# Optimization experiments

Hardware: AMD Instinct MI355X
Metric: run time of the kernel (lower is better)

The kernel has to match this reference:

```python
import jax, jax.numpy as jnp
import numpy as np

N_NODES = 50000
N_EDGES = 600000
DIM = 128
N_LAYERS = 2


def setup_inputs() -> dict:
    key = jax.random.key(0)
    ks = jax.random.split(key, 4)
    x = jax.random.normal(ks[0], (N_NODES, DIM), dtype=jnp.float32)
    edge_index = jax.random.randint(ks[1], (2, N_EDGES), 0, N_NODES, dtype=jnp.int32)
    # xavier_normal-ish scale for transform (fan_in=fan_out=DIM) and gate
    Wt = jax.random.normal(ks[2], (N_LAYERS, DIM, DIM), dtype=jnp.float32) * (1.414 * (2.0 / (2 * DIM)) ** 0.5)
    Wg = jax.random.normal(ks[3], (N_LAYERS, DIM), dtype=jnp.float32) * (1.414 * (2.0 / (DIM + 1)) ** 0.5)
    bt = jnp.zeros((N_LAYERS, DIM), dtype=jnp.float32)
    bg = jnp.zeros((N_LAYERS,), dtype=jnp.float32)
    return {"x": x, "edge_index": edge_index, "Wt": Wt, "bt": bt, "Wg": Wg, "bg": bg}


def _fa_layer(h, row, col, Wt_l, bt_l, Wg_l, bg_l):
    # h: [N, D]. transform
    h = h @ Wt_l.T + bt_l
    n = h.shape[0]
    ones = jnp.ones(row.shape, dtype=h.dtype)
    deg = jnp.clip(jax.ops.segment_sum(ones, row, num_segments=n), 1.0)
    dinv = deg ** -0.5  # [N]
    # per-edge gate on source node features
    g = jnp.tanh(h[row] @ Wg_l + bg_l)  # [E]
    norm = g * dinv[row] * dinv[col]    # [E]
    msg = norm[:, None] * h[row]        # [E, D]
    out = jax.ops.segment_sum(msg, col, num_segments=n)
    return out + h


def reference(x, edge_index, Wt, bt, Wg, bg):
    row, col = edge_index[0], edge_index[1]
    h = x
    for l in range(N_LAYERS):
        h = _fa_layer(h, row, col, Wt[l], bt[l], Wg[l], bg[l])
        h = jax.nn.relu(h)  # dropout p=0 / eval -> identity
    return h
```

## Files before the change

kernel.cpp:

```cpp
#include <hip/hip_runtime.h>
#include <cstdint>
#include <cstddef>

#define DIM 128
#define BM 128
#define NB1 128
#define RBITS 14
#define RSIZE (1 << RBITS)
#define NB2 32
#define NWC 4

typedef __attribute__((ext_vector_type(8))) short bf16x8;
typedef __attribute__((ext_vector_type(16))) float f32x16;

__device__ inline unsigned short f2b(float x) {
    unsigned int u = __float_as_uint(x);
    unsigned int r = (u + 0x7fffu + ((u >> 16) & 1u)) >> 16;
    return (unsigned short)r;
}
__device__ inline float blo(unsigned int u) { return __uint_as_float(u << 16); }
__device__ inline float bhi(unsigned int u) { return __uint_as_float(u & 0xffff0000u); }

__global__ __launch_bounds__(256) void hists_kernel(
    const int* __restrict__ row, const int* __restrict__ col,
    const float* __restrict__ Wt, unsigned short* __restrict__ wbuf,
    int* __restrict__ gcounts, int* __restrict__ counts,
    int E, int ndeg, int nbuk, int bshift)
{
    __shared__ int hs[RSIZE];
    int b = blockIdx.x;
    if (b < ndeg) {
        int r = b / NB2, bi = b % NB2;
        for (int i = threadIdx.x; i < RSIZE; i += 256) hs[i] = 0;
        __syncthreads();
        int chunk = (E + NB2 - 1) / NB2;
        int e0 = bi * chunk, e1 = min(E, e0 + chunk);
        for (int e = e0 + threadIdx.x; e < e1; e += 256) {
            int rv = row[e];
            if ((rv >> RBITS) == r) atomicAdd(&hs[rv & (RSIZE - 1)], 1);
        }
        __syncthreads();
        int* outp = gcounts + (size_t)b * RSIZE;
        for (int i = threadIdx.x; i < RSIZE; i += 256) outp[i] = hs[i];
    } else if (b < ndeg + NB1) {
        int hb = b - ndeg;
        for (int i = threadIdx.x; i < nbuk; i += 256) hs[i] = 0;
        __syncthreads();
        int chunk = (E + NB1 - 1) / NB1;
        int e0 = hb * chunk, e1 = min(E, e0 + chunk);
        for (int e = e0 + threadIdx.x; e < e1; e += 256)
            atomicAdd(&hs[col[e] >> bshift], 1);
        __syncthreads();
        int* outp = counts + (size_t)hb * nbuk;
        for (int i = threadIdx.x; i < nbuk; i += 256) outp[i] = hs[i];
    } else {
        int b2 = b - ndeg - NB1;
#pragma unroll
        for (int k = 0; k < 4; ++k) {
            int idx = b2 * 1024 + k * 256 + threadIdx.x;
            int L = idx >> 11;
            int rem = idx & 2047;
            int r = rem >> 4;
            int cc = rem & 15;
            const float* src = Wt + (size_t)L * DIM * DIM + r * DIM + cc * 8;
            float4 v0 = *(const float4*)(src);
            float4 v1 = *(const float4*)(src + 4);
            unsigned short o[8];
            o[0] = f2b(v0.x); o[1] = f2b(v0.y); o[2] = f2b(v0.z); o[3] = f2b(v0.w);
            o[4] = f2b(v1.x); o[5] = f2b(v1.y); o[6] = f2b(v1.z); o[7] = f2b(v1.w);
            unsigned short* dst = wbuf + (size_t)L * DIM * DIM + r * DIM + (cc ^ (r & 15)) * 8;
            *(int4*)dst = *(const int4*)o;
        }
    }
}

__global__ __launch_bounds__(256) void scan_dinv_kernel(
    int* __restrict__ counts, int* __restrict__ tot,
    const int* __restrict__ gcounts, float* __restrict__ dinv,
    int nbuk, int n, int nscan)
{
    int b = blockIdx.x;
    if (b < nscan) {
        int w = threadIdx.x >> 6;
        int lane = threadIdx.x & 63;
        int t = b * 4 + w;
        if (t >= nbuk) return;
        int c0 = counts[(size_t)(lane * 2) * nbuk + t];
        int c1 = counts[(size_t)(lane * 2 + 1) * nbuk + t];
        int s = c0 + c1;
        int x = s;
#pragma unroll
        for (int d = 1; d < 64; d <<= 1) {
            int y = __shfl_up(x, (unsigned)d, 64);
            if (lane >= d) x += y;
        }
        int excl = x - s;
        counts[(size_t)(lane * 2) * nbuk + t] = excl;
        counts[(size_t)(lane * 2 + 1) * nbuk + t] = excl + c0;
        if (lane == 63) tot[t] = x;
    } else {
        int i = (b - nscan) * 256 + threadIdx.x;
        if (i >= n) return;
        int r = i >> RBITS, bl = i & (RSIZE - 1);
        int s = 0;
        for (int bi = 0; bi < NB2; ++bi)
            s += gcounts[(size_t)(r * NB2 + bi) * RSIZE + bl];
        dinv[i] = rsqrtf((float)max(s, 1));
    }
}

__global__ __launch_bounds__(256) void scatter_kernel(
    const int* __restrict__ row, const int* __restrict__ col,
    const int* __restrict__ bases, const int* __restrict__ tot,
    unsigned int* __restrict__ tmp, int* __restrict__ bstart,
    int E, int nbuk, int bshift)
{
    __shared__ int scanbuf[256];
    __shared__ int bst[1024];
    __shared__ int cur[1024];
    int t = threadIdx.x;
    int v[4];
    int s = 0;
#pragma unroll
    for (int k = 0; k < 4; ++k) {
        int idx = t * 4 + k;
        v[k] = (idx < nbuk) ? tot[idx] : 0;
        s += v[k];
    }
    scanbuf[t] = s;
    __syncthreads();
    for (int d = 1; d < 256; d <<= 1) {
        int y = (t >= d) ? scanbuf[t - d] : 0;
        __syncthreads();
        scanbuf[t] += y;
        __syncthreads();
    }
    int run = scanbuf[t] - s;
#pragma unroll
    for (int k = 0; k < 4; ++k) {
        int idx = t * 4 + k;
        if (idx < nbuk) bst[idx] = run;
        run += v[k];
    }
    __syncthreads();
    const int* mybase = bases + (size_t)blockIdx.x * nbuk;
    for (int i = t; i < nbuk; i += 256) cur[i] = bst[i] + mybase[i];
    if (blockIdx.x == 0) {
        for (int i = t; i < nbuk; i += 256) bstart[i] = bst[i];
        if (t == 0) bstart[nbuk] = E;
    }
    __syncthreads();
    int chunk = (E + NB1 - 1) / NB1;
    int e0 = blockIdx.x * chunk, e1 = min(E, e0 + chunk);
    int rsh = 32 - bshift;
    unsigned int smask = (1u << bshift) - 1u;
    for (int e = e0 + t; e < e1; e += 256) {
        int c = col[e];
        int pos = atomicAdd(&cur[c >> bshift], 1);
        tmp[pos] = (((unsigned int)c & smask) << rsh) | (unsigned int)row[e];
    }
}

__global__ __launch_bounds__(256) void bucket_group_kernel(
    const unsigned int* __restrict__ tmp, const int* __restrict__ bstart,
    int* __restrict__ off, int* __restrict__ csr, int n, int E, int bshift)
{
    __shared__ int subh[4096];
    const int b = blockIdx.x;
    const int tid = threadIdx.x;
    const int subb = 1 << bshift;
    const int rsh = 32 - bshift;
    const unsigned int rmask = (1u << rsh) - 1u;
    int beg = bstart[b], end = bstart[b + 1];

    for (int i = tid; i < subb; i += 256) subh[i] = 0;
    __syncthreads();
    for (int i = beg + tid; i < end; i += 256)
        atomicAdd(&subh[tmp[i] >> rsh], 1);
    __syncthreads();
    if (subb <= 64) {
        if (tid < 64) {
            int v = (tid < subb) ? subh[tid] : 0;
            int x = v;
            for (int d = 1; d < 64; d <<= 1) {
                int y = __shfl_up(x, (unsigned)d, 64);
                if (tid >= d) x += y;
            }
            if (tid < subb) subh[tid] = x - v;
        }
    } else {
        if (tid == 0) {
            int run = 0;
            for (int i = 0; i < subb; ++i) { int c = subh[i]; subh[i] = run; run += c; }
        }
    }
    __syncthreads();
    int c0 = b << bshift;
    for (int i = tid; i < subb; i += 256) {
        int c = c0 + i;
        if (c < n) off[c] = beg + subh[i];
    }
    if (b == gridDim.x - 1 && tid == 0) off[n] = E;
    __syncthreads();
    for (int i = beg + tid; i < end; i += 256) {
        unsigned int v = tmp[i];
        int rank = atomicAdd(&subh[v >> rsh], 1);
        csr[beg + rank] = (int)(v & rmask);
    }
}

template <bool BF16IN>
__global__ __launch_bounds__(256) void transform_kernel(
    const void* __restrict__ hin_v, const unsigned short* __restrict__ wbuf,
    const float* __restrict__ bt, const float* __restrict__ Wg,
    const float* __restrict__ bg, const float* __restrict__ dinv,
    unsigned short* __restrict__ h1b, float* __restrict__ aout, int n)
{
    __shared__ __align__(16) unsigned short h_s[BM * DIM];
    __shared__ __align__(16) unsigned short w_s[DIM * DIM];
    __shared__ float p_s[BM];

    const int tid = threadIdx.x;
    const int node0 = blockIdx.x * BM;
    const int lane = tid & 63;
    const int wv = tid >> 6;

#pragma unroll
    for (int it = 0; it < 8; ++it) {
        int g = it * 256 + tid;
        ((int4*)w_s)[g] = ((const int4*)wbuf)[g];
    }
    if constexpr (BF16IN) {
        const int4* hin = (const int4*)hin_v;
#pragma unroll
        for (int it = 0; it < 8; ++it) {
            int g = it * 256 + tid;
            int r = g >> 4;
            int src = node0 + r;
            if (src >= n) src = n - 1;
            ((int4*)h_s)[g] = hin[(size_t)src * 16 + (g & 15)];
        }
    } else {
        const float* hin = (const float*)hin_v;
#pragma unroll
        for (int it = 0; it < 16; ++it) {
            int g = it * 256 + tid;
            int r = g >> 5;
            int c4 = g & 31;
            int src = node0 + r;
            if (src >= n) src = n - 1;
            float4 hv = *(const float4*)(hin + (size_t)src * DIM + c4 * 4);
            int chunk = (c4 >> 1) ^ (r & 15);
            int base = r * DIM + chunk * 8 + (c4 & 1) * 4;
            h_s[base + 0] = f2b(hv.x); h_s[base + 1] = f2b(hv.y);
            h_s[base + 2] = f2b(hv.z); h_s[base + 3] = f2b(hv.w);
        }
    }
    __syncthreads();

    f32x16 acc[4] = {};
    const int l31 = lane & 31;
    const int asel = lane >> 5;
    const int swz = l31 & 15;
    const unsigned short* ha = h_s + (wv * 32 + l31) * DIM;
#pragma unroll
    for (int ks = 0; ks < 8; ++ks) {
        int ch = ((ks * 2 + asel) ^ swz) * 8;
        bf16x8 av = *(const bf16x8*)(ha + ch);
#pragma unroll
        for (int cf = 0; cf < 4; ++cf) {
            bf16x8 bv = *(const bf16x8*)(w_s + (cf * 32 + l31) * DIM + ch);
            acc[cf] = __builtin_amdgcn_mfma_f32_32x32x16_bf16(av, bv, acc[cf], 0, 0, 0);
        }
    }
    __syncthreads();

    float btc[4], wgc[4];
#pragma unroll
    for (int cf = 0; cf < 4; ++cf) {
        btc[cf] = bt[cf * 32 + l31];
        wgc[cf] = Wg[cf * 32 + l31];
    }
    float p[16];
#pragma unroll
    for (int q = 0; q < 16; ++q) p[q] = 0.0f;
#pragma unroll
    for (int cf = 0; cf < 4; ++cf) {
#pragma unroll
        for (int q = 0; q < 16; ++q) {
            float v = acc[cf][q] + btc[cf];
            p[q] = fmaf(v, wgc[cf], p[q]);
            int row = (q & 3) + 8 * (q >> 2) + 4 * asel;
            h_s[(wv * 32 + row) * DIM + cf * 32 + l31] = f2b(v);
        }
    }
#pragma unroll
    for (int m = 1; m < 32; m <<= 1) {
#pragma unroll
        for (int q = 0; q < 16; ++q) p[q] += __shfl_xor(p[q], m, 64);
    }
    if (l31 == 0) {
#pragma unroll
        for (int q = 0; q < 16; ++q) {
            int row = (q & 3) + 8 * (q >> 2) + 4 * asel;
            p_s[wv * 32 + row] = p[q];
        }
    }
    __syncthreads();

#pragma unroll
    for (int it = 0; it < 8; ++it) {
        int g = it * 256 + tid;
        int r = g >> 4;
        int c = g & 15;
        int4 v = *(const int4*)(h_s + r * DIM + c * 8);
        int dst = node0 + r;
        if (dst < n) *(int4*)(h1b + (size_t)dst * DIM + c * 8) = v;
    }

    if (tid < BM) {
        int node = node0 + tid;
        if (node < n) aout[node] = tanhf(p_s[tid] + bg[0]) * dinv[node];
    }
}

template <bool BF16OUT>
__global__ __launch_bounds__(256) void agg_kernel(
    const int* __restrict__ off, const int* __restrict__ csr_row,
    const float* __restrict__ a, const float* __restrict__ dinv,
    const unsigned short* __restrict__ h1b, void* __restrict__ out_v, int n)
{
    int node = blockIdx.x * 4 + (threadIdx.x >> 6);
    if (node >= n) return;
    int lane = threadIdx.x & 63;
    int beg = off[node], end = off[node + 1];
    const unsigned int* hb = (const unsigned int*)h1b;
    float s0x = 0.f, s0y = 0.f, s1x = 0.f, s1y = 0.f;
    float s2x = 0.f, s2y = 0.f, s3x = 0.f, s3y = 0.f;
    int s = beg;
    for (; s + 4 <= end; s += 4) {
        int r0 = csr_row[s], r1 = csr_row[s + 1], r2 = csr_row[s + 2], r3 = csr_row[s + 3];
        float a0 = a[r0], a1 = a[r1], a2 = a[r2], a3 = a[r3];
        unsigned int u0 = hb[(size_t)r0 * 64 + lane];
        unsigned int u1 = hb[(size_t)r1 * 64 + lane];
        unsigned int u2 = hb[(size_t)r2 * 64 + lane];
        unsigned int u3 = hb[(size_t)r3 * 64 + lane];
        s0x = fmaf(a0, blo(u0), s0x); s0y = fmaf(a0, bhi(u0), s0y);
        s1x = fmaf(a1, blo(u1), s1x); s1y = fmaf(a1, bhi(u1), s1y);
        s2x = fmaf(a2, blo(u2), s2x); s2y = fmaf(a2, bhi(u2), s2y);
        s3x = fmaf(a3, blo(u3), s3x); s3y = fmaf(a3, bhi(u3), s3y);
    }
    for (; s < end; ++s) {
        int r0 = csr_row[s];
        float a0 = a[r0];
        unsigned int u0 = hb[(size_t)r0 * 64 + lane];
        s0x = fmaf(a0, blo(u0), s0x); s0y = fmaf(a0, bhi(u0), s0y);
    }
    float dv = dinv[node];
    unsigned int ur = hb[(size_t)node * 64 + lane];
    float ox = fmaxf(fmaf(dv, s0x + s1x + s2x + s3x, blo(ur)), 0.0f);
    float oy = fmaxf(fmaf(dv, s0y + s1y + s2y + s3y, bhi(ur)), 0.0f);
    if constexpr (BF16OUT) {
        unsigned int pk = (unsigned int)f2b(ox) | ((unsigned int)f2b(oy) << 16);
        int pos = (((lane >> 2) ^ (node & 15)) << 2) + (lane & 3);
        ((unsigned int*)out_v)[(size_t)node * 64 + pos] = pk;
    } else {
        ((float2*)out_v)[(size_t)node * 64 + lane] = make_float2(ox, oy);
    }
}

extern "C" void kernel_launch(void* const* d_in, const int* in_sizes, int n_in,
                              void* d_out, int out_size, void* d_ws, size_t ws_size,
                              hipStream_t stream) {
    const float* x    = (const float*)d_in[0];
    const int*   edge = (const int*)d_in[1];
    const float* Wt   = (const float*)d_in[2];
    const float* bt   = (const float*)d_in[3];
    const float* Wg   = (const float*)d_in[4];
    const float* bg   = (const float*)d_in[5];
    float* out = (float*)d_out;

    const int n = in_sizes[0] / DIM;
    const int E = in_sizes[1] / 2;
    const int* row = edge;
    const int* col = edge + E;

    int bshift = 6;
    while (((n + (1 << bshift) - 1) >> bshift) > 1024) ++bshift;
    const int nbuk = (n + (1 << bshift) - 1) >> bshift;
    const int nr = (n + RSIZE - 1) >> RBITS;
    const int ndeg = nr * NB2;

    char* base = (char*)d_ws;
    size_t o = 0;
    auto carve = [&](size_t bytes) -> void* {
        void* p = base + o;
        o += (bytes + 255) & ~(size_t)255;
        return p;
    };
    unsigned short* h1b  = (unsigned short*)carve((size_t)n * DIM * 2);
    unsigned short* hbuf = (unsigned short*)carve((size_t)n * DIM * 2);
    unsigned short* wbuf = (unsigned short*)carve((size_t)2 * DIM * DIM * 2);
    float* dinv          = (float*)carve((size_t)n * 4);
    float* a             = (float*)carve((size_t)n * 4);
    int*   off           = (int*)carve((size_t)(n + 1) * 4);
    int*   csr           = (int*)carve((size_t)E * 4);
    unsigned int* tmp    = (unsigned int*)carve((size_t)E * 4);
    int*   counts        = (int*)carve((size_t)NB1 * nbuk * 4);
    int*   bstart        = (int*)carve((size_t)(nbuk + 1) * 4);
    int*   tot           = (int*)carve((size_t)nbuk * 4);
    int*   gcounts       = (int*)carve((size_t)ndeg * RSIZE * 4);

    hists_kernel<<<ndeg + NB1 + NWC, 256, 0, stream>>>(
        row, col, Wt, wbuf, gcounts, counts, E, ndeg, nbuk, bshift);
    const int nscan = (nbuk + 3) / 4;
    const int ndinv = (n + 255) / 256;
    scan_dinv_kernel<<<nscan + ndinv, 256, 0, stream>>>(counts, tot, gcounts, dinv,
                                                        nbuk, n, nscan);
    scatter_kernel<<<NB1, 256, 0, stream>>>(row, col, counts, tot, tmp, bstart,
                                            E, nbuk, bshift);
    bucket_group_kernel<<<nbuk, 256, 0, stream>>>(tmp, bstart, off, csr, n, E, bshift);

    const int gt = (n + BM - 1) / BM;
    const int ga = (n + 3) / 4;

    transform_kernel<false><<<gt, 256, 0, stream>>>(
        x, wbuf, bt, Wg, bg, dinv, h1b, a, n);
    agg_kernel<true><<<ga, 256, 0, stream>>>(off, csr, a, dinv, h1b, hbuf, n);

    transform_kernel<true><<<gt, 256, 0, stream>>>(
        hbuf, wbuf + DIM * DIM, bt + DIM, Wg + DIM, bg + 1, dinv, h1b, a, n);
    agg_kernel<false><<<ga, 256, 0, stream>>>(off, csr, a, dinv, h1b, out, n);
}
```

Baseline: 150.0 us.

## Fold layer-1 transform into histogram kernel and defer gate epilogue

The first-layer dense transform now runs as extra blocks of the histogram/weight-conversion kernel. Those blocks convert Wt from fp32 on the fly and store the raw gate pre-activation, since dinv is not yet available at that point. The tanh*dinv gate is finished by extra blocks appended to the scatter kernel. This removes one launch and overlaps the GEMM with the CSR build. Aggregation outputs now use nontemporal stores. The cost is a larger shared-memory footprint for all blocks in the merged kernel, which may reduce histogram-block occupancy.

```diff
diff --git a/kernel.cpp b/kernel.cpp
--- a/kernel.cpp
+++ b/kernel.cpp
@@ -21,216 +21,47 @@
 __device__ inline float blo(unsigned int u) { return __uint_as_float(u << 16); }
 __device__ inline float bhi(unsigned int u) { return __uint_as_float(u & 0xffff0000u); }
 
-__global__ __launch_bounds__(256) void hists_kernel(
-    const int* __restrict__ row, const int* __restrict__ col,
-    const float* __restrict__ Wt, unsigned short* __restrict__ wbuf,
-    int* __restrict__ gcounts, int* __restrict__ counts,
-    int E, int ndeg, int nbuk, int bshift)
+struct GArgs {
+    const float* x; const int* row; const int* col;
+    const float* Wt; const float* bt; const float* Wg; const float* bg;
+    unsigned short* wbuf; unsigned short* h1b; unsigned short* hbuf;
+    float* dinv; float* a; float* praw; float* out;
+    int* off; int* csr; unsigned int* tmp; int* counts; int* bstart; int* tot;
+    int* gcounts;
+    int n, E, nbuk, bshift, ndeg, nscan, ndinv, gt, ga;
+};
+
+__device__ void transform_body(bool bf16in, bool wfromf32, const void* hin_v,
+    const float* WtL, const unsigned short* wbufL,
+    const float* btL, const float* WgL, float bgL,
+    const float* dinv, unsigned short* h1b, float* aout, bool fullepi,
+    int n, int tb, unsigned short* h_s, unsigned short* w_s, float* p_s)
 {
-    __shared__ int hs[RSIZE];
-    int b = blockIdx.x;
-    if (b < ndeg) {
-        int r = b / NB2, bi = b % NB2;
-        for (int i = threadIdx.x; i < RSIZE; i += 256) hs[i] = 0;
-        __syncthreads();
-        int chunk = (E + NB2 - 1) / NB2;
-        int e0 = bi * chunk, e1 = min(E, e0 + chunk);
-        for (int e = e0 + threadIdx.x; e < e1; e += 256) {
-            int rv = row[e];
-            if ((rv >> RBITS) == r) atomicAdd(&hs[rv & (RSIZE - 1)], 1);
-        }
-        __syncthreads();
-        int* outp = gcounts + (size_t)b * RSIZE;
-        for (int i = threadIdx.x; i < RSIZE; i += 256) outp[i] = hs[i];
-    } else if (b < ndeg + NB1) {
-        int hb = b - ndeg;
-        for (int i = threadIdx.x; i < nbuk; i += 256) hs[i] = 0;
-        __syncthreads();
-        int chunk = (E + NB1 - 1) / NB1;
-        int e0 = hb * chunk, e1 = min(E, e0 + chunk);
-        for (int e = e0 + threadIdx.x; e < e1; e += 256)
-            atomicAdd(&hs[col[e] >> bshift], 1);
-        __syncthreads();
-        int* outp = counts + (size_t)hb * nbuk;
-        for (int i = threadIdx.x; i < nbuk; i += 256) outp[i] = hs[i];
-    } else {
-        int b2 = b - ndeg - NB1;
-#pragma unroll
-        for (int k = 0; k < 4; ++k) {
-            int idx = b2 * 1024 + k * 256 + threadIdx.x;
-            int L = idx >> 11;
-            int rem = idx & 2047;
-            int r = rem >> 4;
-            int cc = rem & 15;
-            const float* src = Wt + (size_t)L * DIM * DIM + r * DIM + cc * 8;
-            float4 v0 = *(const float4*)(src);
-            float4 v1 = *(const float4*)(src + 4);
-            unsigned short o[8];
-            o[0] = f2b(v0.x); o[1] = f2b(v0.y); o[2] = f2b(v0.z); o[3] = f2b(v0.w);
-            o[4] = f2b(v1.x); o[5] = f2b(v1.y); o[6] = f2b(v1.z); o[7] = f2b(v1.w);
-            unsigned short* dst = wbuf + (size_t)L * DIM * DIM + r * DIM + (cc ^ (r & 15)) * 8;
-            *(int4*)dst = *(const int4*)o;
-        }
-    }
-}
-
-__global__ __launch_bounds__(256) void scan_dinv_kernel(
-    int* __restrict__ counts, int* __restrict__ tot,
-    const int* __restrict__ gcounts, float* __restrict__ dinv,
-    int nbuk, int n, int nscan)
-{
-    int b = blockIdx.x;
-    if (b < nscan) {
-        int w = threadIdx.x >> 6;
-        int lane = threadIdx.x & 63;
-        int t = b * 4 + w;
-        if (t >= nbuk) return;
-        int c0 = counts[(size_t)(lane * 2) * nbuk + t];
-        int c1 = counts[(size_t)(lane * 2 + 1) * nbuk + t];
-        int s = c0 + c1;
-        int x = s;
-#pragma unroll
-        for (int d = 1; d < 64; d <<= 1) {
-            int y = __shfl_up(x, (unsigned)d, 64);
-            if (lane >= d) x += y;
-        }
-        int excl = x - s;
-        counts[(size_t)(lane * 2) * nbuk + t] = excl;
-        counts[(size_t)(lane * 2 + 1) * nbuk + t] = excl + c0;
-        if (lane == 63) tot[t] = x;
-    } else {
-        int i = (b - nscan) * 256 + threadIdx.x;
-        if (i >= n) return;
-        int r = i >> RBITS, bl = i & (RSIZE - 1);
-        int s = 0;
-        for (int bi = 0; bi < NB2; ++bi)
-            s += gcounts[(size_t)(r * NB2 + bi) * RSIZE + bl];
-        dinv[i] = rsqrtf((float)max(s, 1));
-    }
-}
-
-__global__ __launch_bounds__(256) void scatter_kernel(
-    const int* __restrict__ row, const int* __restrict__ col,
-    const int* __restrict__ bases, const int* __restrict__ tot,
-    unsigned int* __restrict__ tmp, int* __restrict__ bstart,
-    int E, int nbuk, int bshift)
-{
-    __shared__ int scanbuf[256];
-    __shared__ int bst[1024];
-    __shared__ int cur[1024];
-    int t = threadIdx.x;
-    int v[4];
-    int s = 0;
-#pragma unroll
-    for (int k = 0; k < 4; ++k) {
-        int idx = t * 4 + k;
-        v[k] = (idx < nbuk) ? tot[idx] : 0;
-        s += v[k];
-    }
-    scanbuf[t] = s;
-    __syncthreads();
-    for (int d = 1; d < 256; d <<= 1) {
-        int y = (t >= d) ? scanbuf[t - d] : 0;
-        __syncthreads();
-        scanbuf[t] += y;
-        __syncthreads();
-    }
-    int run = scanbuf[t] - s;
-#pragma unroll
-    for (int k = 0; k < 4; ++k) {
-        int idx = t * 4 + k;
-        if (idx < nbuk) bst[idx] = run;
-        run += v[k];
-    }
-    __syncthreads();
-    const int* mybase = bases + (size_t)blockIdx.x * nbuk;
-    for (int i = t; i < nbuk; i += 256) cur[i] = bst[i] + mybase[i];
-    if (blockIdx.x == 0) {
-        for (int i = t; i < nbuk; i += 256) bstart[i] = bst[i];
-        if (t == 0) bstart[nbuk] = E;
-    }
-    __syncthreads();
-    int chunk = (E + NB1 - 1) / NB1;
-    int e0 = blockIdx.x * chunk, e1 = min(E, e0 + chunk);
-    int rsh = 32 - bshift;
-    unsigned int smask = (1u << bshift) - 1u;
-    for (int e = e0 + t; e < e1; e += 256) {
-        int c = col[e];
-        int pos = atomicAdd(&cur[c >> bshift], 1);
-        tmp[pos] = (((unsigned int)c & smask) << rsh) | (unsigned int)row[e];
-    }
-}
-
-__global__ __launch_bounds__(256) void bucket_group_kernel(
-    const unsigned int* __restrict__ tmp, const int* __restrict__ bstart,
-    int* __restrict__ off, int* __restrict__ csr, int n, int E, int bshift)
-{
-    __shared__ int subh[4096];
-    const int b = blockIdx.x;
     const int tid = threadIdx.x;
-    const int subb = 1 << bshift;
-    const int rsh = 32 - bshift;
-    const unsigned int rmask = (1u << rsh) - 1u;
-    int beg = bstart[b], end = bstart[b + 1];
-
-    for (int i = tid; i < subb; i += 256) subh[i] = 0;
-    __syncthreads();
-    for (int i = beg + tid; i < end; i += 256)
-        atomicAdd(&subh[tmp[i] >> rsh], 1);
-    __syncthreads();
-    if (subb <= 64) {
-        if (tid < 64) {
-            int v = (tid < subb) ? subh[tid] : 0;
-            int x = v;
-            for (int d = 1; d < 64; d <<= 1) {
-                int y = __shfl_up(x, (unsigned)d, 64);
-                if (tid >= d) x += y;
-            }
-            if (tid < subb) subh[tid] = x - v;
-        }
-    } else {
-        if (tid == 0) {
-            int run = 0;
-            for (int i = 0; i < subb; ++i) { int c = subh[i]; subh[i] = run; run += c; }
-        }
-    }
-    __syncthreads();
-    int c0 = b << bshift;
-    for (int i = tid; i < subb; i += 256) {
-        int c = c0 + i;
-        if (c < n) off[c] = beg + subh[i];
-    }
-    if (b == gridDim.x - 1 && tid == 0) off[n] = E;
-    __syncthreads();
-    for (int i = beg + tid; i < end; i += 256) {
-        unsigned int v = tmp[i];
-        int rank = atomicAdd(&subh[v >> rsh], 1);
-        csr[beg + rank] = (int)(v & rmask);
-    }
-}
-
-template <bool BF16IN>
-__global__ __launch_bounds__(256) void transform_kernel(
-    const void* __restrict__ hin_v, const unsigned short* __restrict__ wbuf,
-    const float* __restrict__ bt, const float* __restrict__ Wg,
-    const float* __restrict__ bg, const float* __restrict__ dinv,
-    unsigned short* __restrict__ h1b, float* __restrict__ aout, int n)
-{
-    __shared__ __align__(16) unsigned short h_s[BM * DIM];
-    __shared__ __align__(16) unsigned short w_s[DIM * DIM];
-    __shared__ float p_s[BM];
-
-    const int tid = threadIdx.x;
-    const int node0 = blockIdx.x * BM;
+    const int node0 = tb * BM;
     const int lane = tid & 63;
     const int wv = tid >> 6;
 
-#pragma unroll
-    for (int it = 0; it < 8; ++it) {
-        int g = it * 256 + tid;
-        ((int4*)w_s)[g] = ((const int4*)wbuf)[g];
-    }
-    if constexpr (BF16IN) {
+    if (wfromf32) {
+#pragma unroll
+        for (int it = 0; it < 16; ++it) {
+            int g = it * 256 + tid;
+            int r = g >> 5;
+            int c4 = g & 31;
+            int chunk = (c4 >> 1) ^ (r & 15);
+            int base = r * DIM + chunk * 8 + (c4 & 1) * 4;
+            float4 wvv = *(const float4*)(WtL + (size_t)r * DIM + c4 * 4);
+            w_s[base + 0] = f2b(wvv.x); w_s[base + 1] = f2b(wvv.y);
+            w_s[base + 2] = f2b(wvv.z); w_s[base + 3] = f2b(wvv.w);
+        }
+    } else {
+#pragma unroll
+        for (int it = 0; it < 8; ++it) {
+            int g = it * 256 + tid;
+            ((int4*)w_s)[g] = ((const int4*)wbufL)[g];
+        }
+    }
+    if (bf16in) {
         const int4* hin = (const int4*)hin_v;
 #pragma unroll
         for (int it = 0; it < 8; ++it) {
@@ -278,8 +109,8 @@
     float btc[4], wgc[4];
 #pragma unroll
     for (int cf = 0; cf < 4; ++cf) {
-        btc[cf] = bt[cf * 32 + l31];
-        wgc[cf] = Wg[cf * 32 + l31];
+        btc[cf] = btL[cf * 32 + l31];
+        wgc[cf] = WgL[cf * 32 + l31];
     }
     float p[16];
 #pragma unroll
@@ -290,8 +121,8 @@
         for (int q = 0; q < 16; ++q) {
             float v = acc[cf][q] + btc[cf];
             p[q] = fmaf(v, wgc[cf], p[q]);
-            int row = (q & 3) + 8 * (q >> 2) + 4 * asel;
-            h_s[(wv * 32 + row) * DIM + cf * 32 + l31] = f2b(v);
+            int rr = (q & 3) + 8 * (q >> 2) + 4 * asel;
+            h_s[(wv * 32 + rr) * DIM + cf * 32 + l31] = f2b(v);
         }
     }
 #pragma unroll
@@ -302,8 +133,8 @@
     if (l31 == 0) {
 #pragma unroll
         for (int q = 0; q < 16; ++q) {
-            int row = (q & 3) + 8 * (q >> 2) + 4 * asel;
-            p_s[wv * 32 + row] = p[q];
+            int rr = (q & 3) + 8 * (q >> 2) + 4 * asel;
+            p_s[wv * 32 + rr] = p[q];
         }
     }
     __syncthreads();
@@ -320,27 +151,221 @@
 
     if (tid < BM) {
         int node = node0 + tid;
-        if (node < n) aout[node] = tanhf(p_s[tid] + bg[0]) * dinv[node];
-    }
+        if (node < n) {
+            if (fullepi) aout[node] = tanhf(p_s[tid] + bgL) * dinv[node];
+            else         aout[node] = p_s[tid];
+        }
+    }
+}
+
+__global__ __launch_bounds__(256) void mega1_kernel(GArgs A) {
+    __shared__ __align__(16) unsigned char smem[66048];
+    int b = blockIdx.x;
+    if (b < A.ndeg) {
+        int* hs = (int*)smem;
+        int r = b / NB2, bi = b % NB2;
+        for (int i = threadIdx.x; i < RSIZE; i += 256) hs[i] = 0;
+        __syncthreads();
+        int chunk = (A.E + NB2 - 1) / NB2;
+        int e0 = bi * chunk, e1 = min(A.E, e0 + chunk);
+        for (int e = e0 + threadIdx.x; e < e1; e += 256) {
+            int rv = A.row[e];
+            if ((rv >> RBITS) == r) atomicAdd(&hs[rv & (RSIZE - 1)], 1);
+        }
+        __syncthreads();
+        int* outp = A.gcounts + (size_t)b * RSIZE;
+        for (int i = threadIdx.x; i < RSIZE; i += 256) outp[i] = hs[i];
+    } else if (b < A.ndeg + NB1) {
+        int* hs = (int*)smem;
+        int hb = b - A.ndeg;
+        for (int i = threadIdx.x; i < A.nbuk; i += 256) hs[i] = 0;
+        __syncthreads();
+        int chunk = (A.E + NB1 - 1) / NB1;
+        int e0 = hb * chunk, e1 = min(A.E, e0 + chunk);
+        for (int e = e0 + threadIdx.x; e < e1; e += 256)
+            atomicAdd(&hs[A.col[e] >> A.bshift], 1);
+        __syncthreads();
+        int* outp = A.counts + (size_t)hb * A.nbuk;
+        for (int i = threadIdx.x; i < A.nbuk; i += 256) outp[i] = hs[i];
+    } else if (b < A.ndeg + NB1 + NWC) {
+        int b2 = b - A.ndeg - NB1;
+#pragma unroll
+        for (int k = 0; k < 4; ++k) {
+            int idx = b2 * 1024 + k * 256 + threadIdx.x;
+            int L = idx >> 11;
+            int rem = idx & 2047;
+            int r = rem >> 4;
+            int cc = rem & 15;
+            const float* src = A.Wt + (size_t)L * DIM * DIM + r * DIM + cc * 8;
+            float4 v0 = *(const float4*)(src);
+            float4 v1 = *(const float4*)(src + 4);
+            unsigned short o[8];
+            o[0] = f2b(v0.x); o[1] = f2b(v0.y); o[2] = f2b(v0.z); o[3] = f2b(v0.w);
+            o[4] = f2b(v1.x); o[5] = f2b(v1.y); o[6] = f2b(v1.z); o[7] = f2b(v1.w);
+            unsigned short* dst = A.wbuf + (size_t)L * DIM * DIM + r * DIM + (cc ^ (r & 15)) * 8;
+            *(int4*)dst = *(const int4*)o;
+        }
+    } else {
+        int tb = b - (A.ndeg + NB1 + NWC);
+        unsigned short* h_s = (unsigned short*)smem;
+        unsigned short* w_s = h_s + BM * DIM;
+        float* p_s = (float*)(w_s + DIM * DIM);
+        transform_body(false, true, A.x, A.Wt, nullptr, A.bt, A.Wg, 0.0f,
+                       nullptr, A.h1b, A.praw, false, A.n, tb, h_s, w_s, p_s);
+    }
+}
+
+__global__ __launch_bounds__(256) void scan_dinv_kernel(GArgs A) {
+    int b = blockIdx.x;
+    if (b < A.nscan) {
+        int w = threadIdx.x >> 6;
+        int lane = threadIdx.x & 63;
+        int t = b * 4 + w;
+        if (t >= A.nbuk) return;
+        int c0 = A.counts[(size_t)(lane * 2) * A.nbuk + t];
+        int c1 = A.counts[(size_t)(lane * 2 + 1) * A.nbuk + t];
+        int s = c0 + c1;
+        int x = s;
+#pragma unroll
+        for (int d = 1; d < 64; d <<= 1) {
+            int y = __shfl_up(x, (unsigned)d, 64);
+            if (lane >= d) x += y;
+        }
+        int excl = x - s;
+        A.counts[(size_t)(lane * 2) * A.nbuk + t] = excl;
+        A.counts[(size_t)(lane * 2 + 1) * A.nbuk + t] = excl + c0;
+        if (lane == 63) A.tot[t] = x;
+    } else {
+        int i = (b - A.nscan) * 256 + threadIdx.x;
+        if (i >= A.n) return;
+        int r = i >> RBITS, bl = i & (RSIZE - 1);
+        int s = 0;
+        for (int bi = 0; bi < NB2; ++bi)
+            s += A.gcounts[(size_t)(r * NB2 + bi) * RSIZE + bl];
+        A.dinv[i] = rsqrtf((float)max(s, 1));
+    }
+}
+
+__global__ __launch_bounds__(256) void scatter_kernel(GArgs A) {
+    int b = blockIdx.x;
+    int t = threadIdx.x;
+    if (b >= NB1) {
+        int i = (b - NB1) * 256 + t;
+        if (i < A.n) A.a[i] = tanhf(A.praw[i] + A.bg[0]) * A.dinv[i];
+        return;
+    }
+    __shared__ int scanbuf[256];
+    __shared__ int bst[1024];
+    __shared__ int cur[1024];
+    int v[4];
+    int s = 0;
+#pragma unroll
+    for (int k = 0; k < 4; ++k) {
+        int idx = t * 4 + k;
+        v[k] = (idx < A.nbuk) ? A.tot[idx] : 0;
+        s += v[k];
+    }
+    scanbuf[t] = s;
+    __syncthreads();
+    for (int d = 1; d < 256; d <<= 1) {
+        int y = (t >= d) ? scanbuf[t - d] : 0;
+        __syncthreads();
+        scanbuf[t] += y;
+        __syncthreads();
+    }
+    int run = scanbuf[t] - s;
+#pragma unroll
+    for (int k = 0; k < 4; ++k) {
+        int idx = t * 4 + k;
+        if (idx < A.nbuk) bst[idx] = run;
+        run += v[k];
+    }
+    __syncthreads();
+    const int* mybase = A.counts + (size_t)b * A.nbuk;
+    for (int i = t; i < A.nbuk; i += 256) cur[i] = bst[i] + mybase[i];
+    if (b == 0) {
+        for (int i = t; i < A.nbuk; i += 256) A.bstart[i] = bst[i];
+        if (t == 0) A.bstart[A.nbuk] = A.E;
+    }
+    __syncthreads();
+    int chunk = (A.E + NB1 - 1) / NB1;
+    int e0 = b * chunk, e1 = min(A.E, e0 + chunk);
+    int rsh = 32 - A.bshift;
+    unsigned int smask = (1u << A.bshift) - 1u;
+    for (int e = e0 + t; e < e1; e += 256) {
+        int c = A.col[e];
+        int pos = atomicAdd(&cur[c >> A.bshift], 1);
+        A.tmp[pos] = (((unsigned int)c & smask) << rsh) | (unsigned int)A.row[e];
+    }
+}
+
+__global__ __launch_bounds__(256) void bucket_group_kernel(GArgs A) {
+    __shared__ int subh[4096];
+    const int b = blockIdx.x;
+    const int tid = threadIdx.x;
+    const int subb = 1 << A.bshift;
+    const int rsh = 32 - A.bshift;
+    const unsigned int rmask = (1u << rsh) - 1u;
+    int beg = A.bstart[b], end = A.bstart[b + 1];
+
+    for (int i = tid; i < subb; i += 256) subh[i] = 0;
+    __syncthreads();
+    for (int i = beg + tid; i < end; i += 256)
+        atomicAdd(&subh[A.tmp[i] >> rsh], 1);
+    __syncthreads();
+    if (subb <= 64) {
+        if (tid < 64) {
+            int v = (tid < subb) ? subh[tid] : 0;
+            int x = v;
+            for (int d = 1; d < 64; d <<= 1) {
+                int y = __shfl_up(x, (unsigned)d, 64);
+                if (tid >= d) x += y;
+            }
+            if (tid < subb) subh[tid] = x - v;
+        }
+    } else {
+        if (tid == 0) {
+            int run = 0;
+            for (int i = 0; i < subb; ++i) { int c = subh[i]; subh[i] = run; run += c; }
+        }
+    }
+    __syncthreads();
+    int c0 = b << A.bshift;
+    for (int i = tid; i < subb; i += 256) {
+        int c = c0 + i;
+        if (c < A.n) A.off[c] = beg + subh[i];
+    }
+    if (b == (int)gridDim.x - 1 && tid == 0) A.off[A.n] = A.E;
+    __syncthreads();
+    for (int i = beg + tid; i < end; i += 256) {
+        unsigned int v = A.tmp[i];
+        int rank = atomicAdd(&subh[v >> rsh], 1);
+        A.csr[beg + rank] = (int)(v & rmask);
+    }
+}
+
+__global__ __launch_bounds__(256) void t1_kernel(GArgs A) {
+    __shared__ __align__(16) unsigned short h_s[BM * DIM];
+    __shared__ __align__(16) unsigned short w_s[DIM * DIM];
+    __shared__ float p_s[BM];
+    transform_body(true, false, A.hbuf, nullptr, A.wbuf + DIM * DIM,
+                   A.bt + DIM, A.Wg + DIM, A.bg[1], A.dinv, A.h1b, A.a, true,
+                   A.n, blockIdx.x, h_s, w_s, p_s);
 }
 
 template <bool BF16OUT>
-__global__ __launch_bounds__(256) void agg_kernel(
-    const int* __restrict__ off, const int* __restrict__ csr_row,
-    const float* __restrict__ a, const float* __restrict__ dinv,
-    const unsigned short* __restrict__ h1b, void* __restrict__ out_v, int n)
-{
+__global__ __launch_bounds__(256) void agg_kernel(GArgs A, void* out_v) {
     int node = blockIdx.x * 4 + (threadIdx.x >> 6);
-    if (node >= n) return;
+    if (node >= A.n) return;
     int lane = threadIdx.x & 63;
-    int beg = off[node], end = off[node + 1];
-    const unsigned int* hb = (const unsigned int*)h1b;
+    int beg = A.off[node], end = A.off[node + 1];
+    const unsigned int* hb = (const unsigned int*)A.h1b;
     float s0x = 0.f, s0y = 0.f, s1x = 0.f, s1y = 0.f;
     float s2x = 0.f, s2y = 0.f, s3x = 0.f, s3y = 0.f;
     int s = beg;
     for (; s + 4 <= end; s += 4) {
-        int r0 = csr_row[s], r1 = csr_row[s + 1], r2 = csr_row[s + 2], r3 = csr_row[s + 3];
-        float a0 = a[r0], a1 = a[r1], a2 = a[r2], a3 = a[r3];
+        int r0 = A.csr[s], r1 = A.csr[s + 1], r2 = A.csr[s + 2], r3 = A.csr[s + 3];
+        float a0 = A.a[r0], a1 = A.a[r1], a2 = A.a[r2], a3 = A.a[r3];
         unsigned int u0 = hb[(size_t)r0 * 64 + lane];
         unsigned int u1 = hb[(size_t)r1 * 64 + lane];
         unsigned int u2 = hb[(size_t)r2 * 64 + lane];
@@ -351,21 +376,23 @@
         s3x = fmaf(a3, blo(u3), s3x); s3y = fmaf(a3, bhi(u3), s3y);
     }
     for (; s < end; ++s) {
-        int r0 = csr_row[s];
-        float a0 = a[r0];
+        int r0 = A.csr[s];
+        float a0 = A.a[r0];
         unsigned int u0 = hb[(size_t)r0 * 64 + lane];
         s0x = fmaf(a0, blo(u0), s0x); s0y = fmaf(a0, bhi(u0), s0y);
     }
-    float dv = dinv[node];
+    float dv = A.dinv[node];
     unsigned int ur = hb[(size_t)node * 64 + lane];
     float ox = fmaxf(fmaf(dv, s0x + s1x + s2x + s3x, blo(ur)), 0.0f);
     float oy = fmaxf(fmaf(dv, s0y + s1y + s2y + s3y, bhi(ur)), 0.0f);
     if constexpr (BF16OUT) {
         unsigned int pk = (unsigned int)f2b(ox) | ((unsigned int)f2b(oy) << 16);
         int pos = (((lane >> 2) ^ (node & 15)) << 2) + (lane & 3);
-        ((unsigned int*)out_v)[(size_t)node * 64 + pos] = pk;
-    } else {
-        ((float2*)out_v)[(size_t)node * 64 + lane] = make_float2(ox, oy);
+        __builtin_nontemporal_store(pk, (unsigned int*)out_v + (size_t)node * 64 + pos);
+    } else {
+        float* fp = (float*)out_v + ((size_t)node * 64 + lane) * 2;
+        __builtin_nontemporal_store(ox, fp);
+        __builtin_nontemporal_store(oy, fp + 1);
     }
 }
 
@@ -378,12 +405,9 @@
     const float* bt   = (const float*)d_in[3];
     const float* Wg   = (const float*)d_in[4];
     const float* bg   = (const float*)d_in[5];
-    float* out = (float*)d_out;
 
     const int n = in_sizes[0] / DIM;
     const int E = in_sizes[1] / 2;
-    const int* row = edge;
-    const int* col = edge + E;
 
     int bshift = 6;
     while (((n + (1 << bshift) - 1) >> bshift) > 1024) ++bshift;
@@ -398,37 +422,34 @@
         o += (bytes + 255) & ~(size_t)255;
         return p;
     };
-    unsigned short* h1b  = (unsigned short*)carve((size_t)n * DIM * 2);
-    unsigned short* hbuf = (unsigned short*)carve((size_t)n * DIM * 2);
-    unsigned short* wbuf = (unsigned short*)carve((size_t)2 * DIM * DIM * 2);
-    float* dinv          = (float*)carve((size_t)n * 4);
-    float* a             = (float*)carve((size_t)n * 4);
-    int*   off           = (int*)carve((size_t)(n + 1) * 4);
-    int*   csr           = (int*)carve((size_t)E * 4);
-    unsigned int* tmp    = (unsigned int*)carve((size_t)E * 4);
-    int*   counts        = (int*)carve((size_t)NB1 * nbuk * 4);
-    int*   bstart        = (int*)carve((size_t)(nbuk + 1) * 4);
-    int*   tot           = (int*)carve((size_t)nbuk * 4);
-    int*   gcounts       = (int*)carve((size_t)ndeg * RSIZE * 4);
-
-    hists_kernel<<<ndeg + NB1 + NWC, 256, 0, stream>>>(
-        row, col, Wt, wbuf, gcounts, counts, E, ndeg, nbuk, bshift);
-    const int nscan = (nbuk + 3) / 4;
-    const int ndinv = (n + 255) / 256;
-    scan_dinv_kernel<<<nscan + ndinv, 256, 0, stream>>>(counts, tot, gcounts, dinv,
-                                                        nbuk, n, nscan);
-    scatter_kernel<<<NB1, 256, 0, stream>>>(row, col, counts, tot, tmp, bstart,
-                                            E, nbuk, bshift);
-    bucket_group_kernel<<<nbuk, 256, 0, stream>>>(tmp, bstart, off, csr, n, E, bshift);
-
-    const int gt = (n + BM - 1) / BM;
-    const int ga = (n + 3) / 4;
-
-    transform_kernel<false><<<gt, 256, 0, stream>>>(
-        x, wbuf, bt, Wg, bg, dinv, h1b, a, n);
-    agg_kernel<true><<<ga, 256, 0, stream>>>(off, csr, a, dinv, h1b, hbuf, n);
-
-    transform_kernel<true><<<gt, 256, 0, stream>>>(
-        hbuf, wbuf + DIM * DIM, bt + DIM, Wg + DIM, bg + 1, dinv, h1b, a, n);
-    agg_kernel<false><<<ga, 256, 0, stream>>>(off, csr, a, dinv, h1b, out, n);
-}
+    GArgs A;
+    A.x = x; A.row = edge; A.col = edge + E;
+    A.Wt = Wt; A.bt = bt; A.Wg = Wg; A.bg = bg;
+    A.out = (float*)d_out;
+    A.h1b   = (unsigned short*)carve((size_t)n * DIM * 2);
+    A.hbuf  = (unsigned short*)carve((size_t)n * DIM * 2);
+    A.wbuf  = (unsigned short*)carve((size_t)2 * DIM * DIM * 2);
+    A.dinv  = (float*)carve((size_t)n * 4);
+    A.a     = (float*)carve((size_t)n * 4);
+    A.praw  = (float*)carve((size_t)n * 4);
+    A.off   = (int*)carve((size_t)(n + 1) * 4);
+    A.csr   = (int*)carve((size_t)E * 4);
+    A.tmp   = (unsigned int*)carve((size_t)E * 4);
+    A.counts = (int*)carve((size_t)NB1 * nbuk * 4);
+    A.bstart = (int*)carve((size_t)(nbuk + 1) * 4);
+    A.tot    = (int*)carve((size_t)nbuk * 4);
+    A.gcounts = (int*)carve((size_t)ndeg * RSIZE * 4);
+    A.n = n; A.E = E; A.nbuk = nbuk; A.bshift = bshift; A.ndeg = ndeg;
+    A.nscan = (nbuk + 3) / 4;
+    A.ndinv = (n + 255) / 256;
+    A.gt = (n + BM - 1) / BM;
+    A.ga = (n + 3) / 4;
+
+    mega1_kernel<<<ndeg + NB1 + NWC + A.gt, 256, 0, stream>>>(A);
+    scan_dinv_kernel<<<A.nscan + A.ndinv, 256, 0, stream>>>(A);
+    scatter_kernel<<<NB1 + A.ndinv, 256, 0, stream>>>(A);
+    bucket_group_kernel<<<nbuk, 256, 0, stream>>>(A);
+    agg_kernel<true><<<A.ga, 256, 0, stream>>>(A, A.hbuf);
+    t1_kernel<<<A.gt, 256, 0, stream>>>(A);
+    agg_kernel<false><<<A.ga, 256, 0, stream>>>(A, A.out);
+}
```

Measured after the change: 166.9 us. 11.3% more time.

## Pack degree histogram into 16-bit halves and use nontemporal output stores

Applied to the files above, without the earlier changes.

Doubles the per-block row range of the degree histogram (RBITS 14→15) while keeping LDS size fixed by packing two 16-bit counters per 32-bit word. This halves the number of degree-histogram blocks and the partial-count buffer written and re-read when computing dinv. It also switches the aggregation kernel's output writes to nontemporal stores to avoid polluting cache. A 16-bit counter could overflow if a node chunk had more than 65535 edges to one row, which is safe for these random inputs.

```diff
diff --git a/kernel.cpp b/kernel.cpp
--- a/kernel.cpp
+++ b/kernel.cpp
@@ -5,8 +5,9 @@
 #define DIM 128
 #define BM 128
 #define NB1 128
-#define RBITS 14
+#define RBITS 15
 #define RSIZE (1 << RBITS)
+#define HWORDS (RSIZE / 2)
 #define NB2 32
 #define NWC 4
 
@@ -24,24 +25,25 @@
 __global__ __launch_bounds__(256) void hists_kernel(
     const int* __restrict__ row, const int* __restrict__ col,
     const float* __restrict__ Wt, unsigned short* __restrict__ wbuf,
-    int* __restrict__ gcounts, int* __restrict__ counts,
+    unsigned int* __restrict__ gcounts, int* __restrict__ counts,
     int E, int ndeg, int nbuk, int bshift)
 {
-    __shared__ int hs[RSIZE];
+    __shared__ unsigned int hs[HWORDS];
     int b = blockIdx.x;
     if (b < ndeg) {
         int r = b / NB2, bi = b % NB2;
-        for (int i = threadIdx.x; i < RSIZE; i += 256) hs[i] = 0;
+        for (int i = threadIdx.x; i < HWORDS; i += 256) hs[i] = 0;
         __syncthreads();
         int chunk = (E + NB2 - 1) / NB2;
         int e0 = bi * chunk, e1 = min(E, e0 + chunk);
         for (int e = e0 + threadIdx.x; e < e1; e += 256) {
             int rv = row[e];
-            if ((rv >> RBITS) == r) atomicAdd(&hs[rv & (RSIZE - 1)], 1);
-        }
-        __syncthreads();
-        int* outp = gcounts + (size_t)b * RSIZE;
-        for (int i = threadIdx.x; i < RSIZE; i += 256) outp[i] = hs[i];
+            if ((rv >> RBITS) == r)
+                atomicAdd(&hs[(rv & (RSIZE - 1)) >> 1], 1u << ((rv & 1) << 4));
+        }
+        __syncthreads();
+        unsigned int* outp = gcounts + (size_t)b * HWORDS;
+        for (int i = threadIdx.x; i < HWORDS; i += 256) outp[i] = hs[i];
     } else if (b < ndeg + NB1) {
         int hb = b - ndeg;
         for (int i = threadIdx.x; i < nbuk; i += 256) hs[i] = 0;
@@ -49,10 +51,10 @@
         int chunk = (E + NB1 - 1) / NB1;
         int e0 = hb * chunk, e1 = min(E, e0 + chunk);
         for (int e = e0 + threadIdx.x; e < e1; e += 256)
-            atomicAdd(&hs[col[e] >> bshift], 1);
+            atomicAdd(&hs[col[e] >> bshift], 1u);
         __syncthreads();
         int* outp = counts + (size_t)hb * nbuk;
-        for (int i = threadIdx.x; i < nbuk; i += 256) outp[i] = hs[i];
+        for (int i = threadIdx.x; i < nbuk; i += 256) outp[i] = (int)hs[i];
     } else {
         int b2 = b - ndeg - NB1;
 #pragma unroll
@@ -76,7 +78,7 @@
 
 __global__ __launch_bounds__(256) void scan_dinv_kernel(
     int* __restrict__ counts, int* __restrict__ tot,
-    const int* __restrict__ gcounts, float* __restrict__ dinv,
+    const unsigned int* __restrict__ gcounts, float* __restrict__ dinv,
     int nbuk, int n, int nscan)
 {
     int b = blockIdx.x;
@@ -101,11 +103,12 @@
     } else {
         int i = (b - nscan) * 256 + threadIdx.x;
         if (i >= n) return;
-        int r = i >> RBITS, bl = i & (RSIZE - 1);
-        int s = 0;
+        int r = i >> RBITS;
+        int w = (i & (RSIZE - 1)) >> 1, sh = (i & 1) << 4;
+        unsigned int s = 0;
         for (int bi = 0; bi < NB2; ++bi)
-            s += gcounts[(size_t)(r * NB2 + bi) * RSIZE + bl];
-        dinv[i] = rsqrtf((float)max(s, 1));
+            s += (gcounts[(size_t)(r * NB2 + bi) * HWORDS + w] >> sh) & 0xffffu;
+        dinv[i] = rsqrtf((float)max((int)s, 1));
     }
 }
 
@@ -200,7 +203,7 @@
         int c = c0 + i;
         if (c < n) off[c] = beg + subh[i];
     }
-    if (b == gridDim.x - 1 && tid == 0) off[n] = E;
+    if (b == (int)gridDim.x - 1 && tid == 0) off[n] = E;
     __syncthreads();
     for (int i = beg + tid; i < end; i += 256) {
         unsigned int v = tmp[i];
@@ -363,9 +366,11 @@
     if constexpr (BF16OUT) {
         unsigned int pk = (unsigned int)f2b(ox) | ((unsigned int)f2b(oy) << 16);
         int pos = (((lane >> 2) ^ (node & 15)) << 2) + (lane & 3);
-        ((unsigned int*)out_v)[(size_t)node * 64 + pos] = pk;
+        __builtin_nontemporal_store(pk, (unsigned int*)out_v + (size_t)node * 64 + pos);
     } else {
-        ((float2*)out_v)[(size_t)node * 64 + lane] = make_float2(ox, oy);
+        float* fp = (float*)out_v + ((size_t)node * 64 + lane) * 2;
+        __builtin_nontemporal_store(ox, fp);
+        __builtin_nontemporal_store(oy, fp + 1);
     }
 }
 
@@ -409,7 +414,7 @@
     int*   counts        = (int*)carve((size_t)NB1 * nbuk * 4);
     int*   bstart        = (int*)carve((size_t)(nbuk + 1) * 4);
     int*   tot           = (int*)carve((size_t)nbuk * 4);
-    int*   gcounts       = (int*)carve((size_t)ndeg * RSIZE * 4);
+    unsigned int* gcounts = (unsigned int*)carve((size_t)ndeg * HWORDS * 4);
 
     hists_kernel<<<ndeg + NB1 + NWC, 256, 0, stream>>>(
         row, col, Wt, wbuf, gcounts, counts, E, ndeg, nbuk, bshift);
```

Result: no change. 149.6 us, median of 2 (-0.3%).
